# Optimization experiments

Measured on AMD Instinct MI355X. Metric: run time of the kernel, lower is better.

Reference implementation:

```python
import jax, jax.numpy as jnp
import numpy as np

N = 30000        # nodes
E = 480000       # edges (before self-loops)
F_IN = 512       # input feature dim
HID = 64         # per-head hidden dim
HEADS = 4
WIDTH = HID * HEADS  # 256, concat heads
LAYERS = 3
NCLS = 40
NEG_SLOPE = 0.2


def setup_inputs() -> dict:
    key = jax.random.key(0)
    ks = jax.random.split(key, 16)
    def p(k, shape, scale=0.1):
        return jax.random.normal(k, shape, dtype=jnp.float32) * scale
    return {
        "x": jax.random.normal(ks[0], (N, F_IN), dtype=jnp.float32),
        "edge_index": jax.random.randint(ks[1], (2, E), 0, N, dtype=jnp.int32),
        # layer 1: F_IN -> HEADS*HID (concat)
        "W1": p(ks[2], (F_IN, WIDTH)), "as1": p(ks[3], (HEADS, HID)), "ad1": p(ks[4], (HEADS, HID)), "b1": p(ks[5], (WIDTH,)),
        # layer 2: WIDTH -> WIDTH
        "W2": p(ks[6], (WIDTH, WIDTH)), "as2": p(ks[7], (HEADS, HID)), "ad2": p(ks[8], (HEADS, HID)), "b2": p(ks[9], (WIDTH,)),
        # layer 3: WIDTH -> WIDTH
        "W3": p(ks[10], (WIDTH, WIDTH)), "as3": p(ks[11], (HEADS, HID)), "ad3": p(ks[12], (HEADS, HID)), "b3": p(ks[13], (WIDTH,)),
        # JK='cat' output head: WIDTH*LAYERS -> NCLS
        "Wo": p(ks[14], (WIDTH * LAYERS, NCLS)), "bo": p(ks[15], (NCLS,)),
    }


def gat_layer(x, Wm, a_src, a_dst, b, src, dst):
    # PyG GATConv (concat=True, eval mode): h = xW reshaped [N,H,C];
    # e_ij = leaky_relu(a_src.h_j + a_dst.h_i) for edge j->i, softmax over dst groups.
    n = x.shape[0]
    H, C = a_src.shape
    h = (x @ Wm).reshape(n, H, C)                      # [N,H,C]
    es = jnp.sum(h * a_src, axis=-1)                   # [N,H]
    ed = jnp.sum(h * a_dst, axis=-1)                   # [N,H]
    e = jax.nn.leaky_relu(es[src] + ed[dst], NEG_SLOPE)  # [Etot,H]
    m = jax.ops.segment_max(e, dst, num_segments=n)    # stable softmax per dst node
    w = jnp.exp(e - m[dst])
    den = jax.ops.segment_sum(w, dst, num_segments=n)
    alpha = w / den[dst]                               # [Etot,H]
    out = jax.ops.segment_sum(h[src] * alpha[:, :, None], dst, num_segments=n)  # [N,H,C]
    return out.reshape(n, H * C) + b


def reference(x, edge_index, W1, as1, ad1, b1, W2, as2, ad2, b2, W3, as3, ad3, b3, Wo, bo):
    # add self-loops (PyG GATConv default)
    loops = jnp.arange(N, dtype=edge_index.dtype)
    src = jnp.concatenate([edge_index[0], loops])
    dst = jnp.concatenate([edge_index[1], loops])
    # dropout is identity in eval mode
    h1 = jax.nn.relu(gat_layer(x, W1, as1, ad1, b1, src, dst))
    h2 = jax.nn.relu(gat_layer(h1, W2, as2, ad2, b2, src, dst))
    h3 = jax.nn.relu(gat_layer(h2, W3, as3, ad3, b3, src, dst))
    h = jnp.concatenate([h1, h2, h3], axis=-1)         # JK 'cat': [N, WIDTH*LAYERS]
    return h @ Wo + bo                                 # [N, NCLS]
```

## Files before the change

### kernel.cpp

```cpp
#include <hip/hip_runtime.h>

#define N_NODES 30000
#define N_EDGES 480000
#define ETOT    510000
#define F_IN    512
#define WIDTH   256
#define NCLS    40
#define KCAT    768
#define NPAD    48
#define TM      32

typedef __attribute__((ext_vector_type(8))) short short8;
typedef __attribute__((ext_vector_type(4))) float f32x4;

__device__ __forceinline__ unsigned short f2bf(float f){
  unsigned u = __float_as_uint(f);
  u += 0x7fffu + ((u >> 16) & 1u);
  return (unsigned short)(u >> 16);
}
__device__ __forceinline__ float b2f(unsigned short s){
  return __uint_as_float(((unsigned)s) << 16);
}

__device__ __forceinline__ void gload_lds16(const void* g, void* l){
  __builtin_amdgcn_global_load_lds(
      (const __attribute__((address_space(1))) unsigned int*)g,
      (__attribute__((address_space(3))) unsigned int*)l, 16, 0, 0);
}

__global__ void transpose_w_kernel(const float* __restrict__ W, unsigned short* __restrict__ Wt,
                                   int K, int Nc){
  int k = blockIdx.x * blockDim.x + threadIdx.x;
  int n = blockIdx.y;
  if (k < K) Wt[(size_t)n * K + k] = f2bf(W[(size_t)k * Nc + n]);
}

__global__ void transpose_wo_kernel(const float* __restrict__ Wo, unsigned short* __restrict__ WoT){
  int i = blockIdx.x * blockDim.x + threadIdx.x;
  if (i < NPAD * KCAT){
    int c = i / KCAT, k = i - c * KCAT;
    WoT[i] = (c < NCLS) ? f2bf(Wo[(size_t)k * NCLS + c]) : (unsigned short)0;
  }
}

__global__ void zero_kernel(int* __restrict__ p, int n){
  int i = blockIdx.x * blockDim.x + threadIdx.x;
  if (i < n) p[i] = 0;
}

__global__ void hist_kernel(const int* __restrict__ ei, int* __restrict__ counts){
  int e = blockIdx.x * blockDim.x + threadIdx.x;
  if (e < ETOT){
    int d = (e < N_EDGES) ? ei[N_EDGES + e] : (e - N_EDGES);
    atomicAdd(&counts[d], 1);
  }
}

__global__ __launch_bounds__(1024) void scan_kernel(const int* __restrict__ counts,
                                                    int* __restrict__ offsets,
                                                    int* __restrict__ cursor, int n){
  __shared__ int wsum[16];
  int tid = threadIdx.x, lane = tid & 63, wid = tid >> 6;
  int running = 0;
  int nchunks = (n + 1023) >> 10;
  for (int ch = 0; ch < nchunks; ++ch){
    int i = (ch << 10) + tid;
    int v = (i < n) ? counts[i] : 0;
    int x = v;
    #pragma unroll
    for (int off = 1; off < 64; off <<= 1){
      int t = __shfl_up(x, off, 64);
      if (lane >= off) x += t;
    }
    if (lane == 63) wsum[wid] = x;
    __syncthreads();
    if (wid == 0){
      int s = (lane < 16) ? wsum[lane] : 0;
      #pragma unroll
      for (int off = 1; off < 16; off <<= 1){
        int t = __shfl_up(s, off, 64);
        if (lane >= off) s += t;
      }
      if (lane < 16) wsum[lane] = s;
    }
    __syncthreads();
    int waveprefix = (wid > 0) ? wsum[wid - 1] : 0;
    int excl = x - v + waveprefix + running;
    if (i < n){ offsets[i] = excl; cursor[i] = excl; }
    running += wsum[15];
    __syncthreads();
  }
  if (tid == 0) offsets[n] = running;
}

__global__ void scatter_kernel(const int* __restrict__ ei, int* __restrict__ cursor,
                               int* __restrict__ srcs){
  int e = blockIdx.x * blockDim.x + threadIdx.x;
  if (e < ETOT){
    int s, d;
    if (e < N_EDGES){ s = ei[e]; d = ei[N_EDGES + e]; }
    else { s = e - N_EDGES; d = s; }
    int pos = atomicAdd(&cursor[d], 1);
    srcs[pos] = s;
  }
}

template<int K, bool AF32>
__global__ __launch_bounds__(512, AF32 ? 2 : 4)
void gemm_bres_kernel(const void* __restrict__ Araw,
                      const unsigned short* __restrict__ Bt,
                      const float* __restrict__ a_s,
                      const float* __restrict__ a_d,
                      float* __restrict__ esd,
                      unsigned short* __restrict__ hb,
                      int M, int ntiles){
  constexpr int KT = K / 32;
  constexpr int ROWB = K * 2;
  constexpr int ABUF_US = AF32 ? (TM * K) : (2 * TM * K);
  __shared__ unsigned short Abuf[ABUF_US];
  __shared__ unsigned short hstage[TM * 256];
  __shared__ float cmb[2][TM][8];

  int tid = threadIdx.x;
  int lane = tid & 63, w = tid >> 6;
  int l15 = lane & 15, quad = lane >> 4;
  int c0 = w * 32;

  short8 Bf[KT][2];
  #pragma unroll
  for (int kt = 0; kt < KT; ++kt){
    #pragma unroll
    for (int ct = 0; ct < 2; ++ct){
      Bf[kt][ct] = *(const short8*)(Bt + (size_t)(c0 + ct*16 + l15) * K + kt*32 + quad*8);
    }
  }
  float as_v[2], ad_v[2];
  #pragma unroll
  for (int ct = 0; ct < 2; ++ct){
    as_v[ct] = a_s[c0 + ct*16 + l15];
    ad_v[ct] = a_d[c0 + ct*16 + l15];
  }

  int t = blockIdx.x;
  if (t >= ntiles) return;
  int stride = gridDim.x;

  auto dma_stage = [&](int tt, int bufsel){
    unsigned short* bufb = Abuf + bufsel * (TM * K);
    const char* Ab = (const char*)Araw;
    constexpr int NCH = (TM * K * 2) / (512 * 16);
    #pragma unroll
    for (int c = 0; c < NCH; ++c){
      int L = (c * 512 + tid) * 16;
      int row = L / ROWB;
      int colb = L % ROWB;
      int grow = tt * TM + row; if (grow > M - 1) grow = M - 1;
      const char* src = Ab + (size_t)grow * ROWB + (colb ^ ((row & 7) << 4));
      gload_lds16(src, (char*)bufb + L);
    }
  };

  uint4 va[8];
  auto issue_loads = [&](int tt){
    const char* xb = (const char*)Araw;
    #pragma unroll
    for (int i = 0; i < 8; ++i){
      int L32 = (i * 512 + tid) * 16;
      int row = L32 >> 11;
      int colb = L32 & 2047;
      int grow = tt * TM + row; if (grow > M - 1) grow = M - 1;
      va[i] = *(const uint4*)(xb + (size_t)grow * 2048 + colb);
    }
  };
  auto commit_stage = [&](){
    #pragma unroll
    for (int i = 0; i < 8; ++i){
      int ob = (i * 512 + tid) * 8;
      int row = ob >> 10;
      unsigned u0 = (unsigned)f2bf(__uint_as_float(va[i].x)) |
                    ((unsigned)f2bf(__uint_as_float(va[i].y)) << 16);
      unsigned u1 = (unsigned)f2bf(__uint_as_float(va[i].z)) |
                    ((unsigned)f2bf(__uint_as_float(va[i].w)) << 16);
      uint2 uv; uv.x = u0; uv.y = u1;
      *(uint2*)((char*)Abuf + (ob ^ ((row & 7) << 4))) = uv;
    }
  };

  int cur = 0;
  if constexpr (AF32){
    issue_loads(t);
    commit_stage();
  } else {
    dma_stage(t, 0);
  }
  __syncthreads();

  while (true){
    int nxt = t + stride;
    if constexpr (AF32){
      if (nxt < ntiles) issue_loads(nxt);
    } else {
      if (nxt < ntiles) dma_stage(nxt, cur ^ 1);
    }

    const unsigned short* buf = Abuf + (AF32 ? 0 : cur * (TM * K));
    f32x4 acc[2][2];
    #pragma unroll
    for (int s = 0; s < 2; ++s)
      #pragma unroll
      for (int ct = 0; ct < 2; ++ct)
        acc[s][ct] = (f32x4){0.f, 0.f, 0.f, 0.f};

    #pragma unroll
    for (int s = 0; s < 2; ++s){
      int row = s * 16 + l15;
      int swzus = (row & 7) << 3;
      #pragma unroll
      for (int kt = 0; kt < KT; ++kt){
        short8 af = *(const short8*)(buf + row * K + ((kt * 32 + quad * 8) ^ swzus));
        acc[s][0] = __builtin_amdgcn_mfma_f32_16x16x32_bf16(af, Bf[kt][0], acc[s][0], 0, 0, 0);
        acc[s][1] = __builtin_amdgcn_mfma_f32_16x16x32_bf16(af, Bf[kt][1], acc[s][1], 0, 0, 0);
      }
    }

    #pragma unroll
    for (int s = 0; s < 2; ++s){
      #pragma unroll
      for (int r = 0; r < 4; ++r){
        int row = s * 16 + quad * 4 + r;
        #pragma unroll
        for (int ct = 0; ct < 2; ++ct){
          int colb = (c0 + ct * 16 + l15) * 2;
          *(unsigned short*)((char*)hstage + row * 512 + (colb ^ ((row & 7) << 4)))
              = f2bf(acc[s][ct][r]);
        }
        float se = acc[s][0][r] * as_v[0] + acc[s][1][r] * as_v[1];
        float sd = acc[s][0][r] * ad_v[0] + acc[s][1][r] * ad_v[1];
        #pragma unroll
        for (int off = 1; off < 16; off <<= 1){
          se += __shfl_xor(se, off, 64);
          sd += __shfl_xor(sd, off, 64);
        }
        if (l15 == 0){ cmb[0][row][w] = se; cmb[1][row][w] = sd; }
      }
    }
    __syncthreads();

    int r0 = t * TM;
    #pragma unroll
    for (int c = 0; c < 2; ++c){
      int us = (c * 512 + tid) * 8;
      int row = us >> 8;
      int colb = (us & 255) * 2;
      if (r0 + row < M){
        uint4 v = *(const uint4*)((const char*)hstage + row * 512 + (colb ^ ((row & 7) << 4)));
        *(uint4*)(hb + (size_t)(r0 + row) * 256 + (colb >> 1)) = v;
      }
    }
    if (tid < 256){
      int row = tid >> 3, j = tid & 7, hd = j >> 1, sel = j & 1;
      if (r0 + row < M){
        float v = cmb[sel][row][2 * hd] + cmb[sel][row][2 * hd + 1];
        esd[(size_t)(r0 + row) * 8 + sel * 4 + hd] = v;
      }
    }

    if (nxt >= ntiles) break;
    if constexpr (AF32){
      commit_stage();
    }
    __syncthreads();
    if constexpr (!AF32) cur ^= 1;
    t = nxt;
  }
}

__global__ __launch_bounds__(256) void agg_kernel(const int* __restrict__ offsets,
                                                  const int* __restrict__ srcs,
                                                  const float* __restrict__ esd,
                                                  const unsigned short* __restrict__ hb,
                                                  const float* __restrict__ bias,
                                                  unsigned short* __restrict__ hout){
  __shared__ float eLds[8][64][4];
  __shared__ int   sLds[8][64];
  int wid = threadIdx.x >> 6;
  int lane = threadIdx.x & 63;
  int half = lane >> 5, l32 = lane & 31;
  int slot = wid * 2 + half;
  int n = blockIdx.x * 8 + slot;
  int base = offsets[n];
  int deg = offsets[n + 1] - base;
  float4 edv = *(const float4*)(esd + (size_t)n * 8 + 4);

  float m0 = -1e30f, m1 = -1e30f, m2 = -1e30f, m3 = -1e30f;
  for (int i = l32; i < deg; i += 32){
    int s = srcs[base + i];
    float4 ev = *(const float4*)(esd + (size_t)s * 8);
    float e0 = ev.x + edv.x, e1 = ev.y + edv.y, e2 = ev.z + edv.z, e3 = ev.w + edv.w;
    e0 = e0 > 0.f ? e0 : 0.2f * e0;
    e1 = e1 > 0.f ? e1 : 0.2f * e1;
    e2 = e2 > 0.f ? e2 : 0.2f * e2;
    e3 = e3 > 0.f ? e3 : 0.2f * e3;
    if (i < 64){
      sLds[slot][i] = s;
      *(float4*)(&eLds[slot][i][0]) = (float4){e0, e1, e2, e3};
    }
    m0 = fmaxf(m0, e0); m1 = fmaxf(m1, e1); m2 = fmaxf(m2, e2); m3 = fmaxf(m3, e3);
  }
  #pragma unroll
  for (int off = 1; off < 32; off <<= 1){
    m0 = fmaxf(m0, __shfl_xor(m0, off, 64));
    m1 = fmaxf(m1, __shfl_xor(m1, off, 64));
    m2 = fmaxf(m2, __shfl_xor(m2, off, 64));
    m3 = fmaxf(m3, __shfl_xor(m3, off, 64));
  }
  int head = l32 >> 3;
  float mh  = (head == 0) ? m0 : (head == 1) ? m1 : (head == 2) ? m2 : m3;
  float edh = (head == 0) ? edv.x : (head == 1) ? edv.y : (head == 2) ? edv.z : edv.w;

  float2 a0 = {0.f,0.f}, a1 = {0.f,0.f}, a2 = {0.f,0.f}, a3 = {0.f,0.f};
  float den = 0.f;
  const unsigned short* hcol = hb + 8 * l32;
  for (int i = 0; i < deg; i += 8){
    int sidx[8]; float wgt[8];
    #pragma unroll
    for (int u = 0; u < 8; ++u){
      int idx = i + u;
      bool v = idx < deg;
      float le; int s;
      if (idx < 64 || !v){
        int ic = v ? idx : 0;
        if (ic >= 64) ic = 0;
        s  = sLds[slot][ic];
        le = eLds[slot][ic][head];
      } else {
        s = srcs[base + idx];
        float e = esd[(size_t)s * 8 + head] + edh;
        le = e > 0.f ? e : 0.2f * e;
      }
      sidx[u] = s;
      wgt[u] = v ? __expf(le - mh) : 0.f;
    }
    uint4 hv[8];
    #pragma unroll
    for (int u = 0; u < 8; ++u)
      hv[u] = *(const uint4*)(hcol + (size_t)sidx[u] * WIDTH);
    #pragma unroll
    for (int u = 0; u < 8; ++u){
      float wu = wgt[u];
      den += wu;
      a0.x += wu * __uint_as_float(hv[u].x << 16);
      a0.y += wu * __uint_as_float(hv[u].x & 0xffff0000u);
      a1.x += wu * __uint_as_float(hv[u].y << 16);
      a1.y += wu * __uint_as_float(hv[u].y & 0xffff0000u);
      a2.x += wu * __uint_as_float(hv[u].z << 16);
      a2.y += wu * __uint_as_float(hv[u].z & 0xffff0000u);
      a3.x += wu * __uint_as_float(hv[u].w << 16);
      a3.y += wu * __uint_as_float(hv[u].w & 0xffff0000u);
    }
  }
  float inv = 1.0f / den;
  const float* bp = bias + 8 * l32;
  float4 bv0 = *(const float4*)(bp);
  float4 bv1 = *(const float4*)(bp + 4);
  float o0 = fmaxf(a0.x * inv + bv0.x, 0.f);
  float o1 = fmaxf(a0.y * inv + bv0.y, 0.f);
  float o2 = fmaxf(a1.x * inv + bv0.z, 0.f);
  float o3 = fmaxf(a1.y * inv + bv0.w, 0.f);
  float o4 = fmaxf(a2.x * inv + bv1.x, 0.f);
  float o5 = fmaxf(a2.y * inv + bv1.y, 0.f);
  float o6 = fmaxf(a3.x * inv + bv1.z, 0.f);
  float o7 = fmaxf(a3.y * inv + bv1.w, 0.f);
  uint4 o;
  o.x = (unsigned)f2bf(o0) | ((unsigned)f2bf(o1) << 16);
  o.y = (unsigned)f2bf(o2) | ((unsigned)f2bf(o3) << 16);
  o.z = (unsigned)f2bf(o4) | ((unsigned)f2bf(o5) << 16);
  o.w = (unsigned)f2bf(o6) | ((unsigned)f2bf(o7) << 16);
  *(uint4*)(hout + (size_t)n * WIDTH + 8 * l32) = o;
}

__global__ __launch_bounds__(256) void out_gemm_kernel(const unsigned short* __restrict__ h1,
                                                       const unsigned short* __restrict__ h2,
                                                       const unsigned short* __restrict__ h3,
                                                       const unsigned short* __restrict__ WoT,
                                                       const float* __restrict__ bo,
                                                       float* __restrict__ out){
  int tid = threadIdx.x, lane = tid & 63, wid = tid >> 6;
  int l15 = lane & 15, quad = lane >> 4;
  int m0 = blockIdx.x * 64 + 16 * wid;

  f32x4 acc[3];
  #pragma unroll
  for (int t = 0; t < 3; ++t) acc[t] = (f32x4){0.f, 0.f, 0.f, 0.f};

  int arow = m0 + l15; if (arow >= N_NODES) arow = N_NODES - 1;

  #pragma unroll
  for (int part = 0; part < 3; ++part){
    const unsigned short* hp = (part == 0) ? h1 : (part == 1) ? h2 : h3;
    const unsigned short* ap = hp + (size_t)arow * WIDTH;
    #pragma unroll
    for (int k0 = 0; k0 < WIDTH; k0 += 32){
      short8 af = *(const short8*)(ap + k0 + quad * 8);
      int kk = part * WIDTH + k0;
      #pragma unroll
      for (int t = 0; t < 3; ++t){
        short8 bf = *(const short8*)(WoT + (size_t)(16 * t + l15) * KCAT + kk + quad * 8);
        acc[t] = __builtin_amdgcn_mfma_f32_16x16x32_bf16(af, bf, acc[t], 0, 0, 0);
      }
    }
  }

  int r0 = m0 + quad * 4;
  #pragma unroll
  for (int t = 0; t < 3; ++t){
    int col = 16 * t + l15;
    if (col < NCLS){
      float bc = bo[col];
      #pragma unroll
      for (int r = 0; r < 4; ++r){
        int grow = r0 + r;
        if (grow < N_NODES) out[(size_t)grow * NCLS + col] = acc[t][r] + bc;
      }
    }
  }
}

static inline size_t align256(size_t x){ return (x + 255) & ~(size_t)255; }

extern "C" void kernel_launch(void* const* d_in, const int* in_sizes, int n_in,
                              void* d_out, int out_size, void* d_ws, size_t ws_size,
                              hipStream_t stream) {
  const float* x   = (const float*)d_in[0];
  const int*   ei  = (const int*)  d_in[1];
  const float* W1  = (const float*)d_in[2];
  const float* as1 = (const float*)d_in[3];
  const float* ad1 = (const float*)d_in[4];
  const float* b1  = (const float*)d_in[5];
  const float* W2  = (const float*)d_in[6];
  const float* as2 = (const float*)d_in[7];
  const float* ad2 = (const float*)d_in[8];
  const float* b2  = (const float*)d_in[9];
  const float* W3  = (const float*)d_in[10];
  const float* as3 = (const float*)d_in[11];
  const float* ad3 = (const float*)d_in[12];
  const float* b3  = (const float*)d_in[13];
  const float* Wo  = (const float*)d_in[14];
  const float* bo  = (const float*)d_in[15];
  float* out = (float*)d_out;

  char* p = (char*)d_ws;
  auto take = [&](size_t bytes) -> char* { char* cur = p; p += align256(bytes); return cur; };

  unsigned short* Wt1   = (unsigned short*)take((size_t)WIDTH * F_IN * 2);
  unsigned short* Wt2   = (unsigned short*)take((size_t)WIDTH * WIDTH * 2);
  unsigned short* Wt3   = (unsigned short*)take((size_t)WIDTH * WIDTH * 2);
  unsigned short* WoT   = (unsigned short*)take((size_t)NPAD * KCAT * 2);
  unsigned short* hs    = (unsigned short*)take((size_t)N_NODES * WIDTH * 2);
  float*          esd   = (float*)take((size_t)N_NODES * 8 * 4);
  unsigned short* h1b   = (unsigned short*)take((size_t)N_NODES * WIDTH * 2);
  unsigned short* h2b   = (unsigned short*)take((size_t)N_NODES * WIDTH * 2);
  unsigned short* h3b   = (unsigned short*)take((size_t)N_NODES * WIDTH * 2);
  int*            counts  = (int*)take((size_t)N_NODES * 4);
  int*            offsets = (int*)take((size_t)(N_NODES + 1) * 4);
  int*            cursor  = (int*)take((size_t)N_NODES * 4);
  int*            srcs    = (int*)take((size_t)ETOT * 4);

  transpose_w_kernel<<<dim3(F_IN / 256, WIDTH), 256, 0, stream>>>(W1, Wt1, F_IN, WIDTH);
  transpose_w_kernel<<<dim3(1, WIDTH), 256, 0, stream>>>(W2, Wt2, WIDTH, WIDTH);
  transpose_w_kernel<<<dim3(1, WIDTH), 256, 0, stream>>>(W3, Wt3, WIDTH, WIDTH);
  transpose_wo_kernel<<<(NPAD * KCAT + 255) / 256, 256, 0, stream>>>(Wo, WoT);

  zero_kernel<<<(N_NODES + 255) / 256, 256, 0, stream>>>(counts, N_NODES);
  hist_kernel<<<(ETOT + 255) / 256, 256, 0, stream>>>(ei, counts);
  scan_kernel<<<1, 1024, 0, stream>>>(counts, offsets, cursor, N_NODES);
  scatter_kernel<<<(ETOT + 255) / 256, 256, 0, stream>>>(ei, cursor, srcs);

  const int ntiles = (N_NODES + TM - 1) / TM;
  const int agg_grid = N_NODES / 8;
  const int out_grid = (N_NODES + 63) / 64;

  gemm_bres_kernel<F_IN, true><<<256, 512, 0, stream>>>(x, Wt1, as1, ad1, esd, hs, N_NODES, ntiles);
  agg_kernel<<<agg_grid, 256, 0, stream>>>(offsets, srcs, esd, hs, b1, h1b);
  gemm_bres_kernel<WIDTH, false><<<512, 512, 0, stream>>>(h1b, Wt2, as2, ad2, esd, hs, N_NODES, ntiles);
  agg_kernel<<<agg_grid, 256, 0, stream>>>(offsets, srcs, esd, hs, b2, h2b);
  gemm_bres_kernel<WIDTH, false><<<512, 512, 0, stream>>>(h2b, Wt3, as3, ad3, esd, hs, N_NODES, ntiles);
  agg_kernel<<<agg_grid, 256, 0, stream>>>(offsets, srcs, esd, hs, b3, h3b);

  out_gemm_kernel<<<out_grid, 256, 0, stream>>>(h1b, h2b, h3b, WoT, bo, out);
}
```

Measured before the change: 429.3 us.

## Fold attention vectors into extra GEMM columns and use one tile per block

Precomputes W·a_src and W·a_dst per head as eight extra bf16 rows of the transposed weight matrix. The GEMM then produces the attention logits through additional MFMA work split across waves, replacing the shuffle reductions in the epilogue. The persistent, double-buffered tile loop is removed in favour of one 32-row tile per block with a padded LDS staging buffer. The trade-offs are lost load/compute overlap and extra per-block B-fragment loads, and the logits are now computed from bf16-rounded W·a products, which changes precision slightly.

```diff
diff --git a/kernel.cpp b/kernel.cpp
--- a/kernel.cpp
+++ b/kernel.cpp
@@ -9,6 +9,8 @@
 #define KCAT    768
 #define NPAD    48
 #define TM      32
+#define BROWS   272
+#define HST     264
 
 typedef __attribute__((ext_vector_type(8))) short short8;
 typedef __attribute__((ext_vector_type(4))) float f32x4;
@@ -33,6 +35,28 @@
   int k = blockIdx.x * blockDim.x + threadIdx.x;
   int n = blockIdx.y;
   if (k < K) Wt[(size_t)n * K + k] = f2bf(W[(size_t)k * Nc + n]);
+}
+
+__global__ __launch_bounds__(256) void av_kernel(const float* __restrict__ W,
+                                                 const float* __restrict__ a_s,
+                                                 const float* __restrict__ a_d,
+                                                 unsigned short* __restrict__ Bt, int K){
+  int k = blockIdx.x;
+  int tid = threadIdx.x;
+  int h = tid >> 6, lane = tid & 63;
+  float wv = W[(size_t)k * WIDTH + tid];
+  float ps = wv * a_s[tid];
+  float pd = wv * a_d[tid];
+  #pragma unroll
+  for (int off = 32; off; off >>= 1){
+    ps += __shfl_down(ps, off, 64);
+    pd += __shfl_down(pd, off, 64);
+  }
+  if (lane == 0){
+    Bt[(size_t)(256 + h) * K + k] = f2bf(ps);
+    Bt[(size_t)(260 + h) * K + k] = f2bf(pd);
+  }
+  if (tid < 8) Bt[(size_t)(264 + tid) * K + k] = 0;
 }
 
 __global__ void transpose_wo_kernel(const float* __restrict__ Wo, unsigned short* __restrict__ WoT){
@@ -109,70 +133,62 @@
 __global__ __launch_bounds__(512, AF32 ? 2 : 4)
 void gemm_bres_kernel(const void* __restrict__ Araw,
                       const unsigned short* __restrict__ Bt,
-                      const float* __restrict__ a_s,
-                      const float* __restrict__ a_d,
                       float* __restrict__ esd,
                       unsigned short* __restrict__ hb,
-                      int M, int ntiles){
+                      int M){
   constexpr int KT = K / 32;
+  constexpr int KE = KT / 8;
   constexpr int ROWB = K * 2;
-  constexpr int ABUF_US = AF32 ? (TM * K) : (2 * TM * K);
-  __shared__ unsigned short Abuf[ABUF_US];
-  __shared__ unsigned short hstage[TM * 256];
-  __shared__ float cmb[2][TM][8];
+  __shared__ unsigned short Abuf[TM * K];
+  __shared__ unsigned short hstage[TM * HST];
+  __shared__ float cmbE[8][TM][9];
 
   int tid = threadIdx.x;
   int lane = tid & 63, w = tid >> 6;
   int l15 = lane & 15, quad = lane >> 4;
   int c0 = w * 32;
-
-  short8 Bf[KT][2];
-  #pragma unroll
-  for (int kt = 0; kt < KT; ++kt){
-    #pragma unroll
-    for (int ct = 0; ct < 2; ++ct){
-      Bf[kt][ct] = *(const short8*)(Bt + (size_t)(c0 + ct*16 + l15) * K + kt*32 + quad*8);
-    }
-  }
-  float as_v[2], ad_v[2];
-  #pragma unroll
-  for (int ct = 0; ct < 2; ++ct){
-    as_v[ct] = a_s[c0 + ct*16 + l15];
-    ad_v[ct] = a_d[c0 + ct*16 + l15];
-  }
-
-  int t = blockIdx.x;
-  if (t >= ntiles) return;
-  int stride = gridDim.x;
-
-  auto dma_stage = [&](int tt, int bufsel){
-    unsigned short* bufb = Abuf + bufsel * (TM * K);
-    const char* Ab = (const char*)Araw;
-    constexpr int NCH = (TM * K * 2) / (512 * 16);
-    #pragma unroll
-    for (int c = 0; c < NCH; ++c){
-      int L = (c * 512 + tid) * 16;
-      int row = L / ROWB;
-      int colb = L % ROWB;
-      int grow = tt * TM + row; if (grow > M - 1) grow = M - 1;
-      const char* src = Ab + (size_t)grow * ROWB + (colb ^ ((row & 7) << 4));
-      gload_lds16(src, (char*)bufb + L);
-    }
-  };
+  int r0 = blockIdx.x * TM;
 
   uint4 va[8];
-  auto issue_loads = [&](int tt){
+  if constexpr (AF32){
     const char* xb = (const char*)Araw;
     #pragma unroll
     for (int i = 0; i < 8; ++i){
       int L32 = (i * 512 + tid) * 16;
       int row = L32 >> 11;
       int colb = L32 & 2047;
-      int grow = tt * TM + row; if (grow > M - 1) grow = M - 1;
+      int grow = r0 + row; if (grow > M - 1) grow = M - 1;
       va[i] = *(const uint4*)(xb + (size_t)grow * 2048 + colb);
     }
-  };
-  auto commit_stage = [&](){
+  } else {
+    const char* Ab = (const char*)Araw;
+    #pragma unroll
+    for (int c = 0; c < 2; ++c){
+      int L = (c * 512 + tid) * 16;
+      int row = L / ROWB;
+      int colb = L % ROWB;
+      int grow = r0 + row; if (grow > M - 1) grow = M - 1;
+      gload_lds16(Ab + (size_t)grow * ROWB + (colb ^ ((row & 7) << 4)),
+                  (char*)Abuf + L);
+    }
+  }
+
+  short8 Bf[KT][2];
+  #pragma unroll
+  for (int kt = 0; kt < KT; ++kt){
+    #pragma unroll
+    for (int ct = 0; ct < 2; ++ct){
+      Bf[kt][ct] = *(const short8*)(Bt + (size_t)(c0 + ct*16 + l15) * K + kt*32 + quad*8);
+    }
+  }
+  short8 Bfe[KE];
+  #pragma unroll
+  for (int i = 0; i < KE; ++i){
+    int kt = w * KE + i;
+    Bfe[i] = *(const short8*)(Bt + (size_t)(256 + l15) * K + kt*32 + quad*8);
+  }
+
+  if constexpr (AF32){
     #pragma unroll
     for (int i = 0; i < 8; ++i){
       int ob = (i * 512 + tid) * 8;
@@ -184,94 +200,65 @@
       uint2 uv; uv.x = u0; uv.y = u1;
       *(uint2*)((char*)Abuf + (ob ^ ((row & 7) << 4))) = uv;
     }
-  };
-
-  int cur = 0;
-  if constexpr (AF32){
-    issue_loads(t);
-    commit_stage();
-  } else {
-    dma_stage(t, 0);
   }
   __syncthreads();
 
-  while (true){
-    int nxt = t + stride;
-    if constexpr (AF32){
-      if (nxt < ntiles) issue_loads(nxt);
-    } else {
-      if (nxt < ntiles) dma_stage(nxt, cur ^ 1);
-    }
-
-    const unsigned short* buf = Abuf + (AF32 ? 0 : cur * (TM * K));
-    f32x4 acc[2][2];
-    #pragma unroll
-    for (int s = 0; s < 2; ++s)
+  f32x4 acc[2][2];
+  f32x4 eacc[2];
+  #pragma unroll
+  for (int s = 0; s < 2; ++s){
+    acc[s][0] = (f32x4){0.f,0.f,0.f,0.f};
+    acc[s][1] = (f32x4){0.f,0.f,0.f,0.f};
+    eacc[s]   = (f32x4){0.f,0.f,0.f,0.f};
+  }
+  #pragma unroll
+  for (int s = 0; s < 2; ++s){
+    int row = s * 16 + l15;
+    int swzus = (row & 7) << 3;
+    const unsigned short* base = Abuf + row * K;
+    #pragma unroll
+    for (int kt = 0; kt < KT; ++kt){
+      short8 af = *(const short8*)(base + ((kt*32 + quad*8) ^ swzus));
+      acc[s][0] = __builtin_amdgcn_mfma_f32_16x16x32_bf16(af, Bf[kt][0], acc[s][0], 0, 0, 0);
+      acc[s][1] = __builtin_amdgcn_mfma_f32_16x16x32_bf16(af, Bf[kt][1], acc[s][1], 0, 0, 0);
+    }
+    #pragma unroll
+    for (int i = 0; i < KE; ++i){
+      int kt = w * KE + i;
+      short8 af = *(const short8*)(base + ((kt*32 + quad*8) ^ swzus));
+      eacc[s] = __builtin_amdgcn_mfma_f32_16x16x32_bf16(af, Bfe[i], eacc[s], 0, 0, 0);
+    }
+  }
+
+  #pragma unroll
+  for (int s = 0; s < 2; ++s){
+    #pragma unroll
+    for (int r = 0; r < 4; ++r){
+      int row = s * 16 + quad * 4 + r;
+      hstage[row * HST + c0 + l15]      = f2bf(acc[s][0][r]);
+      hstage[row * HST + c0 + 16 + l15] = f2bf(acc[s][1][r]);
+      if (l15 < 8) cmbE[w][row][l15] = eacc[s][r];
+    }
+  }
+  __syncthreads();
+
+  #pragma unroll
+  for (int p2 = 0; p2 < 2; ++p2){
+    int us = (p2 * 512 + tid) * 8;
+    int row = us >> 8, col = us & 255;
+    if (r0 + row < M){
+      uint4 v = *(const uint4*)(&hstage[row * HST + col]);
+      *(uint4*)(hb + (size_t)(r0 + row) * WIDTH + col) = v;
+    }
+  }
+  if (tid < 256){
+    int row = tid >> 3, j = tid & 7;
+    if (r0 + row < M){
+      float v = 0.f;
       #pragma unroll
-      for (int ct = 0; ct < 2; ++ct)
-        acc[s][ct] = (f32x4){0.f, 0.f, 0.f, 0.f};
-
-    #pragma unroll
-    for (int s = 0; s < 2; ++s){
-      int row = s * 16 + l15;
-      int swzus = (row & 7) << 3;
-      #pragma unroll
-      for (int kt = 0; kt < KT; ++kt){
-        short8 af = *(const short8*)(buf + row * K + ((kt * 32 + quad * 8) ^ swzus));
-        acc[s][0] = __builtin_amdgcn_mfma_f32_16x16x32_bf16(af, Bf[kt][0], acc[s][0], 0, 0, 0);
-        acc[s][1] = __builtin_amdgcn_mfma_f32_16x16x32_bf16(af, Bf[kt][1], acc[s][1], 0, 0, 0);
-      }
-    }
-
-    #pragma unroll
-    for (int s = 0; s < 2; ++s){
-      #pragma unroll
-      for (int r = 0; r < 4; ++r){
-        int row = s * 16 + quad * 4 + r;
-        #pragma unroll
-        for (int ct = 0; ct < 2; ++ct){
-          int colb = (c0 + ct * 16 + l15) * 2;
-          *(unsigned short*)((char*)hstage + row * 512 + (colb ^ ((row & 7) << 4)))
-              = f2bf(acc[s][ct][r]);
-        }
-        float se = acc[s][0][r] * as_v[0] + acc[s][1][r] * as_v[1];
-        float sd = acc[s][0][r] * ad_v[0] + acc[s][1][r] * ad_v[1];
-        #pragma unroll
-        for (int off = 1; off < 16; off <<= 1){
-          se += __shfl_xor(se, off, 64);
-          sd += __shfl_xor(sd, off, 64);
-        }
-        if (l15 == 0){ cmb[0][row][w] = se; cmb[1][row][w] = sd; }
-      }
-    }
-    __syncthreads();
-
-    int r0 = t * TM;
-    #pragma unroll
-    for (int c = 0; c < 2; ++c){
-      int us = (c * 512 + tid) * 8;
-      int row = us >> 8;
-      int colb = (us & 255) * 2;
-      if (r0 + row < M){
-        uint4 v = *(const uint4*)((const char*)hstage + row * 512 + (colb ^ ((row & 7) << 4)));
-        *(uint4*)(hb + (size_t)(r0 + row) * 256 + (colb >> 1)) = v;
-      }
-    }
-    if (tid < 256){
-      int row = tid >> 3, j = tid & 7, hd = j >> 1, sel = j & 1;
-      if (r0 + row < M){
-        float v = cmb[sel][row][2 * hd] + cmb[sel][row][2 * hd + 1];
-        esd[(size_t)(r0 + row) * 8 + sel * 4 + hd] = v;
-      }
-    }
-
-    if (nxt >= ntiles) break;
-    if constexpr (AF32){
-      commit_stage();
-    }
-    __syncthreads();
-    if constexpr (!AF32) cur ^= 1;
-    t = nxt;
+      for (int ww = 0; ww < 8; ++ww) v += cmbE[ww][row][j];
+      esd[(size_t)(r0 + row) * 8 + j] = v;
+    }
   }
 }
 
@@ -452,9 +439,9 @@
   char* p = (char*)d_ws;
   auto take = [&](size_t bytes) -> char* { char* cur = p; p += align256(bytes); return cur; };
 
-  unsigned short* Wt1   = (unsigned short*)take((size_t)WIDTH * F_IN * 2);
-  unsigned short* Wt2   = (unsigned short*)take((size_t)WIDTH * WIDTH * 2);
-  unsigned short* Wt3   = (unsigned short*)take((size_t)WIDTH * WIDTH * 2);
+  unsigned short* Wt1   = (unsigned short*)take((size_t)BROWS * F_IN * 2);
+  unsigned short* Wt2   = (unsigned short*)take((size_t)BROWS * WIDTH * 2);
+  unsigned short* Wt3   = (unsigned short*)take((size_t)BROWS * WIDTH * 2);
   unsigned short* WoT   = (unsigned short*)take((size_t)NPAD * KCAT * 2);
   unsigned short* hs    = (unsigned short*)take((size_t)N_NODES * WIDTH * 2);
   float*          esd   = (float*)take((size_t)N_NODES * 8 * 4);
@@ -469,6 +456,9 @@
   transpose_w_kernel<<<dim3(F_IN / 256, WIDTH), 256, 0, stream>>>(W1, Wt1, F_IN, WIDTH);
   transpose_w_kernel<<<dim3(1, WIDTH), 256, 0, stream>>>(W2, Wt2, WIDTH, WIDTH);
   transpose_w_kernel<<<dim3(1, WIDTH), 256, 0, stream>>>(W3, Wt3, WIDTH, WIDTH);
+  av_kernel<<<F_IN, 256, 0, stream>>>(W1, as1, ad1, Wt1, F_IN);
+  av_kernel<<<WIDTH, 256, 0, stream>>>(W2, as2, ad2, Wt2, WIDTH);
+  av_kernel<<<WIDTH, 256, 0, stream>>>(W3, as3, ad3, Wt3, WIDTH);
   transpose_wo_kernel<<<(NPAD * KCAT + 255) / 256, 256, 0, stream>>>(Wo, WoT);
 
   zero_kernel<<<(N_NODES + 255) / 256, 256, 0, stream>>>(counts, N_NODES);
@@ -480,11 +470,11 @@
   const int agg_grid = N_NODES / 8;
   const int out_grid = (N_NODES + 63) / 64;
 
-  gemm_bres_kernel<F_IN, true><<<256, 512, 0, stream>>>(x, Wt1, as1, ad1, esd, hs, N_NODES, ntiles);
+  gemm_bres_kernel<F_IN, true><<<ntiles, 512, 0, stream>>>(x, Wt1, esd, hs, N_NODES);
   agg_kernel<<<agg_grid, 256, 0, stream>>>(offsets, srcs, esd, hs, b1, h1b);
-  gemm_bres_kernel<WIDTH, false><<<512, 512, 0, stream>>>(h1b, Wt2, as2, ad2, esd, hs, N_NODES, ntiles);
+  gemm_bres_kernel<WIDTH, false><<<ntiles, 512, 0, stream>>>(h1b, Wt2, esd, hs, N_NODES);
   agg_kernel<<<agg_grid, 256, 0, stream>>>(offsets, srcs, esd, hs, b2, h2b);
-  gemm_bres_kernel<WIDTH, false><<<512, 512, 0, stream>>>(h2b, Wt3, as3, ad3, esd, hs, N_NODES, ntiles);
+  gemm_bres_kernel<WIDTH, false><<<ntiles, 512, 0, stream>>>(h2b, Wt3, esd, hs, N_NODES);
   agg_kernel<<<agg_grid, 256, 0, stream>>>(offsets, srcs, esd, hs, b3, h3b);
 
   out_gemm_kernel<<<out_grid, 256, 0, stream>>>(h1b, h2b, h3b, WoT, bo, out);
```

New measurement: 422.4 us. No clear change (-1.6%).
